# Kernel tuning notes

Measured on AMD Instinct MI355X. Metric: run time of the kernel, lower is better.

## Reference

```python
import jax, jax.numpy as jnp
import numpy as np

B, T, D = 2048, 200, 64
H1, H2 = 128, 64
NEG_INF = jnp.float32(-(2.0**32) + 1.0)


def setup_inputs() -> dict:
    key = jax.random.key(0)
    ks = jax.random.split(key, 10)
    query = jax.random.normal(ks[0], (B, D), dtype=jnp.float32)
    k = jax.random.normal(ks[1], (B, T, D), dtype=jnp.float32)
    v = jax.random.normal(ks[2], (B, T, D), dtype=jnp.float32)
    mask = jax.random.randint(ks[3], (B, T), 0, 2, dtype=jnp.int32)
    # Deep_layer params: concat width 4*D -> H1 -> H2 -> 1
    s1 = 1.0 / np.sqrt(4 * D)
    s2 = 1.0 / np.sqrt(H1)
    s3 = 1.0 / np.sqrt(H2)
    W1 = jax.random.normal(ks[4], (4 * D, H1), dtype=jnp.float32) * s1
    b1 = jnp.zeros((H1,), dtype=jnp.float32)
    W2 = jax.random.normal(ks[5], (H1, H2), dtype=jnp.float32) * s2
    b2 = jnp.zeros((H2,), dtype=jnp.float32)
    Wo = jax.random.normal(ks[6], (H2, 1), dtype=jnp.float32) * s3
    bo = jnp.zeros((1,), dtype=jnp.float32)
    return {"query": query, "key": k, "value": v, "mask": mask,
            "W1": W1, "b1": b1, "W2": W2, "b2": b2, "Wo": Wo, "bo": bo}


def reference(query, key, value, mask, W1, b1, W2, b2, Wo, bo):
    b, t, d = key.shape
    q = jnp.broadcast_to(query[:, None, :], (b, t, d))          # tile query over T
    emb = jnp.concatenate([q, key, q - key, q * key], axis=-1)  # [B,T,4D]
    h = jax.nn.relu(jnp.einsum('btf,fh->bth', emb, W1) + b1)    # [B,T,H1]
    h = jax.nn.relu(jnp.einsum('bth,hk->btk', h, W2) + b2)      # [B,T,H2]
    score = (jnp.einsum('btk,ko->bto', h, Wo) + bo)[..., 0]     # [B,T]
    score = jnp.where(mask == 0, NEG_INF, score)
    attn = jax.nn.softmax(score, axis=-1)                       # [B,T]
    out = jnp.einsum('bt,btd->bd', attn, value)                 # [B,D]
    return out
```

## Files before the change

kernel.cpp:

```cpp
#include <hip/hip_runtime.h>
#include <hip/hip_bf16.h>
#include <cstdint>
#include <cstddef>

#define NB 2048
#define NT 200
#define ND 64
#define NH1 128
#define NH2 64
#define NTILES 7
#define NTP 224

typedef __bf16 bf16x8 __attribute__((ext_vector_type(8)));
typedef float f32x4 __attribute__((ext_vector_type(4)));

#define MFMA16(A, Bv, C) __builtin_amdgcn_mfma_f32_16x16x32_bf16((A), (Bv), (C), 0, 0, 0)

union BF8u { __bf16 b[8]; bf16x8 v; uint4 u4; };

template<int N>
__device__ __forceinline__ float row_ror_add(float v) {
    int r = __builtin_amdgcn_update_dpp(0, __builtin_bit_cast(int, v),
                                        0x120 | N, 0xF, 0xF, false);
    return v + __builtin_bit_cast(float, r);
}

__device__ __forceinline__ void bar_sync() {
    __builtin_amdgcn_sched_barrier(0);
    asm volatile("s_waitcnt lgkmcnt(0)" ::: "memory");
    __builtin_amdgcn_s_barrier();
    __builtin_amdgcn_sched_barrier(0);
}

__global__ void prep_kernel(const float* __restrict__ W1, const float* __restrict__ W2,
                            float* __restrict__ Qp, float* __restrict__ AbT,
                            float* __restrict__ PT, __bf16* __restrict__ W2t) {
    int tid = blockIdx.x * blockDim.x + threadIdx.x;
    if (tid < 64 * NH1) {
        int c = tid >> 7, j = tid & 127;
        Qp[tid] = W1[c * NH1 + j] + W1[(128 + c) * NH1 + j];
        int jj = tid >> 6, cc = tid & 63;
        AbT[tid] = W1[(64 + cc) * NH1 + jj] - W1[(128 + cc) * NH1 + jj];
        PT[tid]  = W1[(192 + cc) * NH1 + jj];
        int j2 = tid >> 7, k = tid & 127;
        W2t[tid] = (__bf16)W2[k * NH2 + j2];
    }
}

__global__ __launch_bounds__(256, 4)
void attn_main(const float* __restrict__ query, const float* __restrict__ key,
               const float* __restrict__ value, const int* __restrict__ mask,
               const float* __restrict__ b1, const float* __restrict__ b2,
               const float* __restrict__ Wo,
               const float* __restrict__ Qp, const float* __restrict__ AbT,
               const float* __restrict__ PT, const __bf16* __restrict__ W2t,
               float* __restrict__ out)
{
    __shared__ __align__(16) char smem[30976];
    auto KHI0 = (__bf16(*)[72])(smem);
    auto KHI1 = (__bf16(*)[72])(smem + 4608);
    auto H10  = (__bf16(*)[136])(smem + 9216);
    auto H11  = (__bf16(*)[136])(smem + 17920);
    auto SP   = (float(*)[NTP])(smem + 26624);
    float* QS  = (float*)(smem + 30208);
    float* QHS = (float*)(smem + 30464);
    float* SCORES = (float*)(smem);
    auto REDS = (float(*)[72])(smem + 9216);

    const int b = blockIdx.x;
    const int tid = threadIdx.x;
    const int lane = tid & 63;
    const int wave = tid >> 6;
    const int jn = lane & 15;
    const int g4 = lane >> 4;
    const int g8 = g4 * 8;

    const int r_st = tid >> 3;
    const int c0   = (tid & 7) * 8;
    const float* kp_base = key + (size_t)b * NT * ND + c0;
    float4 pf[2][2];

    {
        const float* kp0 = kp_base + (size_t)r_st * ND;
        pf[0][0] = *(const float4*)(kp0);
        pf[0][1] = *(const float4*)(kp0 + 4);
        const float* kp1 = kp_base + (size_t)(32 + r_st) * ND;
        pf[1][0] = *(const float4*)(kp1);
        pf[1][1] = *(const float4*)(kp1 + 4);
    }

    if (tid < ND) QS[tid] = query[(size_t)b * ND + tid];
    int mk = 0;
    if (tid < NT) mk = mask[(size_t)b * NT + tid];
    bar_sync();

    if (tid < NH1) {
        float a0 = 0.f, a1 = 0.f, a2 = 0.f, a3 = 0.f;
        #pragma unroll
        for (int c = 0; c < ND; c += 4) {
            a0 = fmaf(QS[c],     Qp[c * NH1 + tid],       a0);
            a1 = fmaf(QS[c + 1], Qp[(c + 1) * NH1 + tid], a1);
            a2 = fmaf(QS[c + 2], Qp[(c + 2) * NH1 + tid], a2);
            a3 = fmaf(QS[c + 3], Qp[(c + 3) * NH1 + tid], a3);
        }
        QHS[tid] = b1[tid] + ((a0 + a1) + (a2 + a3));
    }

    bf16x8 g1_bhi[2][2], g1_blo[2][2];
    const int jown = wave * 32;
    #pragma unroll
    for (int n = 0; n < 2; ++n) {
        const int j = jown + n * 16 + jn;
        #pragma unroll
        for (int kk = 0; kk < 2; ++kk) {
            const float* ab = AbT + j * ND + kk * 32 + g8;
            const float* pt = PT  + j * ND + kk * 32 + g8;
            float4 a0 = *(const float4*)ab, a1 = *(const float4*)(ab + 4);
            float4 p0 = *(const float4*)pt, p1 = *(const float4*)(pt + 4);
            const float va[8] = {a0.x,a0.y,a0.z,a0.w,a1.x,a1.y,a1.z,a1.w};
            const float vp[8] = {p0.x,p0.y,p0.z,p0.w,p1.x,p1.y,p1.z,p1.w};
            BF8u vh, vl;
            #pragma unroll
            for (int e = 0; e < 8; ++e) {
                const int c = kk * 32 + g8 + e;
                float v = fmaf(QS[c], vp[e], va[e]);
                __bf16 hi = (__bf16)v;
                vh.b[e] = hi;
                vl.b[e] = (__bf16)(v - (float)hi);
            }
            g1_bhi[n][kk] = vh.v;
            g1_blo[n][kk] = vl.v;
        }
    }
    bf16x8 g2_w[4];
    {
        const int j2 = wave * 16 + jn;
        #pragma unroll
        for (int kk = 0; kk < 4; ++kk)
            g2_w[kk] = *(const bf16x8*)(W2t + j2 * NH1 + kk * 32 + g8);
    }
    bar_sync();
    const float qh0 = QHS[jown + jn];
    const float qh1 = QHS[jown + 16 + jn];
    const float b2j = b2[wave * 16 + jn];
    const float woj = Wo[wave * 16 + jn];

    f32x4 accc[2][2];
    #pragma unroll
    for (int ti = 0; ti <= NTILES; ++ti) {
        __bf16 (*KCUR)[72]   = (ti & 1) ? KHI1 : KHI0;
        __bf16 (*H1CUR)[136] = ((ti + 1) & 1) ? H11 : H10;

        if (ti < NTILES) {
            const int bi = ti & 1;
            const float vals[8] = {pf[bi][0].x, pf[bi][0].y, pf[bi][0].z, pf[bi][0].w,
                                   pf[bi][1].x, pf[bi][1].y, pf[bi][1].z, pf[bi][1].w};
            BF8u ph;
            #pragma unroll
            for (int i = 0; i < 8; ++i) ph.b[i] = (__bf16)vals[i];
            *(uint4*)(&KCUR[r_st][c0]) = ph.u4;
        }
        if (ti > 0) {
            #pragma unroll
            for (int mt = 0; mt < 2; ++mt)
            #pragma unroll
            for (int n = 0; n < 2; ++n) {
                const float qhj = n ? qh1 : qh0;
                const int j = jown + n * 16 + jn;
                #pragma unroll
                for (int r = 0; r < 4; ++r)
                    H1CUR[mt * 16 + g4 * 4 + r][j] =
                        (__bf16)fmaxf(accc[mt][n][r] + qhj, 0.f);
            }
        }
        bar_sync();

        if (ti + 2 < NTILES) {
            const int bi = ti & 1;
            int t = (ti + 2) * 32 + r_st;
            t = t < NT ? t : NT - 1;
            const float* kp = kp_base + (size_t)t * ND;
            pf[bi][0] = *(const float4*)(kp);
            pf[bi][1] = *(const float4*)(kp + 4);
        }
        if (ti < NTILES) {
            #pragma unroll
            for (int mt = 0; mt < 2; ++mt) {
                const int arow = mt * 16 + jn;
                const bf16x8 a0 = *(const bf16x8*)(&KCUR[arow][g8]);
                const bf16x8 a1 = *(const bf16x8*)(&KCUR[arow][32 + g8]);
                #pragma unroll
                for (int n = 0; n < 2; ++n) {
                    f32x4 ac = {0.f, 0.f, 0.f, 0.f};
                    ac = MFMA16(a0, g1_bhi[n][0], ac);
                    ac = MFMA16(a1, g1_bhi[n][1], ac);
                    ac = MFMA16(a0, g1_blo[n][0], ac);
                    ac = MFMA16(a1, g1_blo[n][1], ac);
                    accc[mt][n] = ac;
                }
            }
        }
        if (ti > 0) {
            const int t0 = (ti - 1) * 32;
            #pragma unroll
            for (int mt = 0; mt < 2; ++mt) {
                const int arow = mt * 16 + jn;
                const bf16x8 h0v = *(const bf16x8*)(&H1CUR[arow][g8]);
                const bf16x8 h1v = *(const bf16x8*)(&H1CUR[arow][32 + g8]);
                const bf16x8 h2v = *(const bf16x8*)(&H1CUR[arow][64 + g8]);
                const bf16x8 h3v = *(const bf16x8*)(&H1CUR[arow][96 + g8]);
                f32x4 cA = {0.f,0.f,0.f,0.f}, cB = {0.f,0.f,0.f,0.f};
                cA = MFMA16(h0v, g2_w[0], cA);
                cB = MFMA16(h1v, g2_w[1], cB);
                cA = MFMA16(h2v, g2_w[2], cA);
                cB = MFMA16(h3v, g2_w[3], cB);
                #pragma unroll
                for (int r = 0; r < 4; ++r) {
                    float v = fmaxf(cA[r] + cB[r] + b2j, 0.f) * woj;
                    v = row_ror_add<8>(v);
                    v = row_ror_add<4>(v);
                    v = row_ror_add<2>(v);
                    v = row_ror_add<1>(v);
                    if (jn == 0) SP[wave][t0 + mt * 16 + g4 * 4 + r] = v;
                }
            }
        }
    }

    const int tg = tid >> 4;
    const int dq = tid & 15;
    const float* vbase = value + (size_t)b * NT * ND + dq * 4;
    const float4 vv0 = *(const float4*)(vbase + (size_t)tg * ND);
    const float4 vv1 = *(const float4*)(vbase + (size_t)(tg + 16) * ND);

    bar_sync();

    if (tid < NTP) {
        const float sc = SP[0][tid] + SP[1][tid] + SP[2][tid] + SP[3][tid];
        SCORES[tid] = (tid < NT && mk != 0) ? __expf(sc) : 0.f;
    }
    bar_sync();

    {
        const float e0 = SCORES[tg], e1 = SCORES[tg + 16];
        float oa0 = fmaf(e1, vv1.x, e0 * vv0.x);
        float oa1 = fmaf(e1, vv1.y, e0 * vv0.y);
        float oa2 = fmaf(e1, vv1.z, e0 * vv0.z);
        float oa3 = fmaf(e1, vv1.w, e0 * vv0.w);
        float den = e0 + e1;
        #pragma unroll 4
        for (int t = tg + 32; t < NT; t += 16) {
            const float e = SCORES[t];
            const float4 v4 = *(const float4*)(vbase + (size_t)t * ND);
            oa0 = fmaf(e, v4.x, oa0); oa1 = fmaf(e, v4.y, oa1);
            oa2 = fmaf(e, v4.z, oa2); oa3 = fmaf(e, v4.w, oa3);
            den += e;
        }
        REDS[tg][dq*4+0] = oa0; REDS[tg][dq*4+1] = oa1;
        REDS[tg][dq*4+2] = oa2; REDS[tg][dq*4+3] = oa3;
        if (dq == 0) REDS[tg][64] = den;
    }
    bar_sync();

    if (tid < ND) {
        float s = 0.f, den = 0.f;
        #pragma unroll
        for (int g = 0; g < 16; ++g) { s += REDS[g][tid]; den += REDS[g][64]; }
        out[(size_t)b * ND + tid] = s / den;
    }
}

extern "C" void kernel_launch(void* const* d_in, const int* in_sizes, int n_in,
                              void* d_out, int out_size, void* d_ws, size_t ws_size,
                              hipStream_t stream) {
    const float* query = (const float*)d_in[0];
    const float* key   = (const float*)d_in[1];
    const float* value = (const float*)d_in[2];
    const int*   maskp = (const int*)d_in[3];
    const float* W1    = (const float*)d_in[4];
    const float* b1    = (const float*)d_in[5];
    const float* W2    = (const float*)d_in[6];
    const float* b2    = (const float*)d_in[7];
    const float* Wo    = (const float*)d_in[8];
    float* out = (float*)d_out;

    float* Qp  = (float*)d_ws;
    float* AbT = Qp + 64 * NH1;
    float* PT  = AbT + NH1 * ND;
    __bf16* W2t = (__bf16*)(PT + NH1 * ND);

    prep_kernel<<<32, 256, 0, stream>>>(W1, W2, Qp, AbT, PT, W2t);
    attn_main<<<NB, 256, 0, stream>>>(query, key, value, maskp, b1, b2, Wo,
                                      Qp, AbT, PT, W2t, out);
}
```

Baseline: 56.60 us.

## Fuse softmax-weighted value accumulation into the tile loop with prefetched value rows

Moves the exp/mask and value-weighted accumulation from a separate tail phase into the main tile loop. Each iteration prefetches the value rows for the previous tile and accumulates the tile before that, so global value loads overlap the MFMA work. The mask is stored as a float array in shared memory, and the SCORES buffer and one barrier are removed. This adds register pressure (value prefetch and accumulators live across the loop) and relies on SP entries for a tile being complete two iterations later, which depends on the loop's existing barriers.

After: 87.22 us. 54.1% more time.

```diff
diff --git a/kernel.cpp b/kernel.cpp
--- a/kernel.cpp
+++ b/kernel.cpp
@@ -56,16 +56,16 @@
                const float* __restrict__ PT, const __bf16* __restrict__ W2t,
                float* __restrict__ out)
 {
-    __shared__ __align__(16) char smem[30976];
+    __shared__ __align__(16) char smem[31872];
     auto KHI0 = (__bf16(*)[72])(smem);
     auto KHI1 = (__bf16(*)[72])(smem + 4608);
     auto H10  = (__bf16(*)[136])(smem + 9216);
     auto H11  = (__bf16(*)[136])(smem + 17920);
     auto SP   = (float(*)[NTP])(smem + 26624);
-    float* QS  = (float*)(smem + 30208);
-    float* QHS = (float*)(smem + 30464);
-    float* SCORES = (float*)(smem);
-    auto REDS = (float(*)[72])(smem + 9216);
+    float* MASKF = (float*)(smem + 30208);
+    float* QS  = (float*)(smem + 31104);
+    float* QHS = (float*)(smem + 31360);
+    auto REDS = (float(*)[72])(smem);
 
     const int b = blockIdx.x;
     const int tid = threadIdx.x;
@@ -74,6 +74,8 @@
     const int jn = lane & 15;
     const int g4 = lane >> 4;
     const int g8 = g4 * 8;
+    const int tg = tid >> 4;
+    const int dq = tid & 15;
 
     const int r_st = tid >> 3;
     const int c0   = (tid & 7) * 8;
@@ -90,8 +92,7 @@
     }
 
     if (tid < ND) QS[tid] = query[(size_t)b * ND + tid];
-    int mk = 0;
-    if (tid < NT) mk = mask[(size_t)b * NT + tid];
+    if (tid < NTP) MASKF[tid] = (tid < NT && mask[(size_t)b * NT + tid] != 0) ? 1.f : 0.f;
     bar_sync();
 
     if (tid < NH1) {
@@ -144,6 +145,10 @@
     const float qh1 = QHS[jown + 16 + jn];
     const float b2j = b2[wave * 16 + jn];
     const float woj = Wo[wave * 16 + jn];
+
+    const float* vbase = value + (size_t)b * NT * ND + dq * 4;
+    float4 vv0{}, vv1{};
+    float oa0 = 0.f, oa1 = 0.f, oa2 = 0.f, oa3 = 0.f, den = 0.f;
 
     f32x4 accc[2][2];
     #pragma unroll
@@ -225,48 +230,49 @@
                 }
             }
         }
-    }
-
-    const int tg = tid >> 4;
-    const int dq = tid & 15;
-    const float* vbase = value + (size_t)b * NT * ND + dq * 4;
-    const float4 vv0 = *(const float4*)(vbase + (size_t)tg * ND);
-    const float4 vv1 = *(const float4*)(vbase + (size_t)(tg + 16) * ND);
+        if (ti >= 2) {
+            const int r0 = (ti - 2) * 32 + tg, r1 = r0 + 16;
+            const float s0 = SP[0][r0] + SP[1][r0] + SP[2][r0] + SP[3][r0];
+            const float s1 = SP[0][r1] + SP[1][r1] + SP[2][r1] + SP[3][r1];
+            const float e0 = MASKF[r0] * __expf(s0);
+            const float e1 = MASKF[r1] * __expf(s1);
+            oa0 = fmaf(e0, vv0.x, fmaf(e1, vv1.x, oa0));
+            oa1 = fmaf(e0, vv0.y, fmaf(e1, vv1.y, oa1));
+            oa2 = fmaf(e0, vv0.z, fmaf(e1, vv1.z, oa2));
+            oa3 = fmaf(e0, vv0.w, fmaf(e1, vv1.w, oa3));
+            den += e0 + e1;
+        }
+        if (ti >= 1) {
+            int t0v = (ti - 1) * 32 + tg;      t0v = t0v < NT ? t0v : NT - 1;
+            int t1v = (ti - 1) * 32 + tg + 16; t1v = t1v < NT ? t1v : NT - 1;
+            vv0 = *(const float4*)(vbase + (size_t)t0v * ND);
+            vv1 = *(const float4*)(vbase + (size_t)t1v * ND);
+        }
+    }
 
     bar_sync();
-
-    if (tid < NTP) {
-        const float sc = SP[0][tid] + SP[1][tid] + SP[2][tid] + SP[3][tid];
-        SCORES[tid] = (tid < NT && mk != 0) ? __expf(sc) : 0.f;
-    }
+    {
+        const int r0 = (NTILES - 1) * 32 + tg, r1 = r0 + 16;
+        const float s0 = SP[0][r0] + SP[1][r0] + SP[2][r0] + SP[3][r0];
+        const float s1 = SP[0][r1] + SP[1][r1] + SP[2][r1] + SP[3][r1];
+        const float e0 = MASKF[r0] * __expf(s0);
+        const float e1 = MASKF[r1] * __expf(s1);
+        oa0 = fmaf(e0, vv0.x, fmaf(e1, vv1.x, oa0));
+        oa1 = fmaf(e0, vv0.y, fmaf(e1, vv1.y, oa1));
+        oa2 = fmaf(e0, vv0.z, fmaf(e1, vv1.z, oa2));
+        oa3 = fmaf(e0, vv0.w, fmaf(e1, vv1.w, oa3));
+        den += e0 + e1;
+    }
+    REDS[tg][dq*4+0] = oa0; REDS[tg][dq*4+1] = oa1;
+    REDS[tg][dq*4+2] = oa2; REDS[tg][dq*4+3] = oa3;
+    if (dq == 0) REDS[tg][64] = den;
     bar_sync();
 
-    {
-        const float e0 = SCORES[tg], e1 = SCORES[tg + 16];
-        float oa0 = fmaf(e1, vv1.x, e0 * vv0.x);
-        float oa1 = fmaf(e1, vv1.y, e0 * vv0.y);
-        float oa2 = fmaf(e1, vv1.z, e0 * vv0.z);
-        float oa3 = fmaf(e1, vv1.w, e0 * vv0.w);
-        float den = e0 + e1;
-        #pragma unroll 4
-        for (int t = tg + 32; t < NT; t += 16) {
-            const float e = SCORES[t];
-            const float4 v4 = *(const float4*)(vbase + (size_t)t * ND);
-            oa0 = fmaf(e, v4.x, oa0); oa1 = fmaf(e, v4.y, oa1);
-            oa2 = fmaf(e, v4.z, oa2); oa3 = fmaf(e, v4.w, oa3);
-            den += e;
-        }
-        REDS[tg][dq*4+0] = oa0; REDS[tg][dq*4+1] = oa1;
-        REDS[tg][dq*4+2] = oa2; REDS[tg][dq*4+3] = oa3;
-        if (dq == 0) REDS[tg][64] = den;
-    }
-    bar_sync();
-
     if (tid < ND) {
-        float s = 0.f, den = 0.f;
+        float s = 0.f, d = 0.f;
         #pragma unroll
-        for (int g = 0; g < 16; ++g) { s += REDS[g][tid]; den += REDS[g][64]; }
-        out[(size_t)b * ND + tid] = s / den;
+        for (int g = 0; g < 16; ++g) { s += REDS[g][tid]; d += REDS[g][64]; }
+        out[(size_t)b * ND + tid] = s / d;
     }
 }
 
```
